# Kernel tuning notes

Hardware: AMD Instinct MI355X
Metric: run time of the kernel (lower is better)

Reference implementation:

```python
import jax, jax.numpy as jnp
import numpy as np

HEADS = 8
DIM_HEAD = 64
NB_FEATURES = 266
EPS = 1e-4


def softmax_kernel(data, projection, is_query):
    # data: (b, h, n, d); projection: (m, d)
    dn = data.shape[-1] ** -0.25                       # data normalizer d^{-1/4}
    ratio = projection.shape[0] ** -0.5                # m^{-1/2}
    dd = jnp.einsum('bhnd,md->bhnm', dn * data, projection)
    diag = (jnp.sum(data * data, axis=-1, keepdims=True) * 0.5) * (dn * dn)
    stab = jnp.max(dd, axis=-1, keepdims=True) if is_query else jnp.max(dd)
    return ratio * (jnp.exp(dd - diag - stab) + EPS)


def linear_attention(q, k, v):
    # q,k: (b,h,n,m) kernel features; v: (b,h,n,d)
    k_sum = k.sum(axis=-2)                                   # (b,h,m)
    D_inv = 1.0 / jnp.einsum('bhnm,bhm->bhn', q, k_sum)      # (b,h,n)
    context = jnp.einsum('bhnm,bhnd->bhmd', k, v)            # (b,h,m,d)
    return jnp.einsum('bhmd,bhnm,bhn->bhnd', context, q, D_inv)


def reference(x, W_qkv, W_out, projection, f):
    B, N, dim = x.shape
    h, dh = HEADS, DIM_HEAD
    qkv = x @ W_qkv                                          # (B,N,3*h*dh)
    q, k, v = jnp.split(qkv, 3, axis=-1)
    to_bh = lambda t: t.reshape(B, N, h, dh).transpose(0, 2, 1, 3).reshape(B * h, N, dh)
    q, k, v = to_bh(q), to_bh(k), to_bh(v)
    q = q * (dh ** -0.5)
    cls_q, q_ = q[:, :1], q[:, 1:]
    cls_k, k_ = k[:, :1], k[:, 1:]
    cls_v, v_ = v[:, :1], v[:, 1:]
    # cls token attends to ALL tokens with exact softmax attention
    sim = jnp.einsum('bid,bjd->bij', cls_q, k)
    cls_out = jnp.einsum('bij,bjd->bid', jax.nn.softmax(sim, axis=-1), v)
    # space attention regroup: 'b (f n) d -> (b f) n d'
    n_sp = (N - 1) // f
    grp = lambda t: t.reshape(B * h * f, n_sp, dh)
    q_, k_, v_ = grp(q_), grp(k_), grp(v_)
    # broadcast cls k/v to each group: 'b () d -> (b r) () d', r = f
    k_ = jnp.concatenate([jnp.repeat(cls_k, f, axis=0), k_], axis=1)  # (B*h*f, n_sp+1, dh)
    v_ = jnp.concatenate([jnp.repeat(cls_v, f, axis=0), v_], axis=1)
    # '(b h) f d -> b h f d'
    sh = lambda t: t.reshape(-1, h, t.shape[1], dh)
    qp = softmax_kernel(sh(q_), projection, True)
    kp = softmax_kernel(sh(k_), projection, False)
    out = linear_attention(qp, kp, sh(v_))                   # (-1, h, n_sp, dh)
    out = out.reshape(B * h, f * n_sp, dh)                   # '(b f) n d -> b (f n) d'
    out = jnp.concatenate([cls_out, out], axis=1)            # (B*h, N, dh)
    out = out.reshape(B, h, N, dh).transpose(0, 2, 1, 3).reshape(B, N, h * dh)
    return out @ W_out


def setup_inputs():
    key = jax.random.key(0)
    ks = jax.random.split(key, 3)
    B, F, S, dim = 8, 16, 196, 512
    N = 1 + F * S
    dh, m = DIM_HEAD, NB_FEATURES
    x = jax.random.normal(ks[0], (B, N, dim), dtype=jnp.float32)
    W_qkv = jax.random.normal(ks[1], (dim, 3 * dim), dtype=jnp.float32) * (dim ** -0.5)
    W_out = jax.random.normal(ks[2], (dim, dim), dtype=jnp.float32) * (dim ** -0.5)
    # gaussian orthogonal random matrix (scaling=0): QR blocks, chi-norm row scales
    rng = np.random.default_rng(0)
    blocks = []
    for _ in range(m // dh):
        qm, _ = np.linalg.qr(rng.standard_normal((dh, dh)))
        blocks.append(qm.T)
    rem = m - (m // dh) * dh
    if rem > 0:
        qm, _ = np.linalg.qr(rng.standard_normal((dh, dh)))
        blocks.append(qm.T[:rem])
    proj = np.concatenate(blocks, axis=0)
    multiplier = np.linalg.norm(rng.standard_normal((m, dh)), axis=1)
    projection = jnp.asarray(multiplier[:, None] * proj, dtype=jnp.float32)
    return {"x": x, "W_qkv": W_qkv, "W_out": W_out, "projection": projection, "f": F}
```

## Files before the change

### kernel.cpp

```cpp
#include <hip/hip_runtime.h>
#include <hip/hip_bf16.h>

namespace {

typedef __bf16 bf16x8 __attribute__((ext_vector_type(8)));
typedef float  f32x4  __attribute__((ext_vector_type(4)));
typedef unsigned short ushort8 __attribute__((ext_vector_type(8)));
typedef unsigned int u32;

constexpr int NTOK  = 3137;
constexpr int NH    = 8;
constexpr int DH    = 64;
constexpr int BH    = 64;
constexpr int MROWS = 8 * NTOK;
constexpr int NROWS = BH * NTOK;
constexpr int MF    = 266;
constexpr int MPK   = 320;
constexpr int MC    = 288;
constexpr int MS    = 320;
constexpr int NMAXB = (NROWS + 255) / 256;
constexpr int NCH   = 13;
constexpr int NBQKV = 197 * 12;
constexpr int NBOUT = 197 * 4;

constexpr float DN     = 0.35355339059327379f;
constexpr float HDN2   = 0.0625f;
constexpr float RATIO  = 0.0613139368f;
constexpr float EPSV   = 1.0e-4f;
constexpr float QSCALE = 0.125f;

__device__ __forceinline__ int swz64(int r, int c)  { return (r << 6) + (c ^ ((r & 7) << 3)); }
__device__ __forceinline__ int swz320(int r, int c) { return r * 320 + (c ^ ((r & 7) << 3)); }

__device__ __forceinline__ int xcdchunk(int bid, int nb) {
  const int q = nb >> 3, r = nb & 7;
  const int xcd = bid & 7, slot = bid >> 3;
  return (xcd < r ? xcd * (q + 1) : r * (q + 1) + (xcd - r) * q) + slot;
}

__device__ __forceinline__ float b2f(unsigned short u) {
  union { unsigned int i; float f; } cv;
  cv.i = ((unsigned int)u) << 16;
  return cv.f;
}
__device__ __forceinline__ unsigned short f2b(float f) {
  __hip_bfloat16 h = __float2bfloat16(f);
  union { __hip_bfloat16 h; unsigned short u; } cv;
  cv.h = h;
  return cv.u;
}
__device__ __forceinline__ unsigned int pk2(float a, float b) {
  return (unsigned int)f2b(a) | ((unsigned int)f2b(b) << 16);
}
__device__ __forceinline__ u32 fenc(float f) {
  u32 u = __float_as_uint(f);
  return (u & 0x80000000u) ? ~u : (u | 0x80000000u);
}
__device__ __forceinline__ float fdec(u32 u) {
  return __uint_as_float((u & 0x80000000u) ? (u ^ 0x80000000u) : ~u);
}
__device__ __forceinline__ void gload16(const void* g, void* l) {
  __builtin_amdgcn_global_load_lds(
      (const __attribute__((address_space(1))) u32*)g,
      (__attribute__((address_space(3))) u32*)l, 16, 0, 0);
}

__global__ __launch_bounds__(256) void k_projb(
    const float* __restrict__ proj, unsigned short* __restrict__ projb,
    u32* __restrict__ gmaxu)
{
  const int idx = (blockIdx.x * 256 + threadIdx.x) * 8;
  if (idx < MPK * 64) {
    const int m = idx >> 6, c0 = idx & 63;
    uint4 u;
    if (m < MF) {
      const float* src = proj + (size_t)m * 64 + c0;
      const float4 f0 = *(const float4*)src;
      const float4 f1 = *(const float4*)(src + 4);
      u.x = pk2(f0.x, f0.y); u.y = pk2(f0.z, f0.w);
      u.z = pk2(f1.x, f1.y); u.w = pk2(f1.z, f1.w);
    } else {
      u = uint4{0, 0, 0, 0};
    }
    *(uint4*)&projb[swz64(m, c0)] = u;
  }
  if (blockIdx.x == 0 && threadIdx.x == 0) *gmaxu = 0u;
}

__global__ __launch_bounds__(256) void k_cvt(
    const float* __restrict__ src, unsigned short* __restrict__ dst, int n8)
{
  const int i = blockIdx.x * 256 + threadIdx.x;
  if (i < n8) {
    const float4 f0 = *(const float4*)(src + (size_t)i * 8);
    const float4 f1 = *(const float4*)(src + (size_t)i * 8 + 4);
    uint4 u;
    u.x = pk2(f0.x, f0.y); u.y = pk2(f0.z, f0.w);
    u.z = pk2(f1.x, f1.y); u.w = pk2(f1.z, f1.w);
    *(uint4*)(dst + (size_t)i * 8) = u;
  }
}

__global__ __launch_bounds__(256) void k_tconv(
    const float* __restrict__ src, unsigned short* __restrict__ dst,
    int R, int C)
{
  __shared__ float tile[64][65];
  const int cb = blockIdx.x * 64, rb = blockIdx.y * 64;
  const int tid = threadIdx.x;
  const int tr = tid >> 4, tc4 = (tid & 15) * 4;
  #pragma unroll
  for (int i = 0; i < 4; ++i) {
    const int r = tr + i * 16;
    const float4 f = *(const float4*)(src + (size_t)(rb + r) * C + cb + tc4);
    tile[r][tc4 + 0] = f.x; tile[r][tc4 + 1] = f.y;
    tile[r][tc4 + 2] = f.z; tile[r][tc4 + 3] = f.w;
  }
  __syncthreads();
  #pragma unroll
  for (int i = 0; i < 4; ++i) {
    const int wrow = tr + i * 16;
    uint2 u;
    u.x = pk2(tile[tc4 + 0][wrow], tile[tc4 + 1][wrow]);
    u.y = pk2(tile[tc4 + 2][wrow], tile[tc4 + 3][wrow]);
    *(uint2*)&dst[(size_t)(cb + wrow) * R + rb + tc4] = u;
  }
}

__global__ __launch_bounds__(256) void k_qkv(
    const unsigned short* __restrict__ xb,
    const unsigned short* __restrict__ wT,
    unsigned short* __restrict__ qb, unsigned short* __restrict__ kb,
    unsigned short* __restrict__ vb)
{
  __shared__ alignas(16) unsigned short As[128 * 64];
  __shared__ alignas(16) unsigned short Bs[128 * 64];
  const int lid = xcdchunk(blockIdx.x, NBQKV);
  const int bm = lid / 12, bn = lid % 12;
  const int tid = threadIdx.x;
  const int lane = tid & 63, wid = tid >> 6;
  const int wr = wid >> 1, wc = wid & 1;
  const int row0 = bm * 128, col0 = bn * 128;
  const int l15 = lane & 15, l4 = lane >> 4;
  const int lr = lane >> 3;
  const int srcChunk = (lane & 7) ^ lr;

  const unsigned short* aRow[4];
  const unsigned short* bRow[4];
  #pragma unroll
  for (int j = 0; j < 4; ++j) {
    int gr = row0 + wid * 32 + j * 8 + lr;
    if (gr >= MROWS) gr = MROWS - 1;
    aRow[j] = xb + (size_t)gr * 512 + srcChunk * 8;
    bRow[j] = wT + (size_t)(col0 + wid * 32 + j * 8 + lr) * 512 + srcChunk * 8;
  }

  f32x4 acc[4][4];
  #pragma unroll
  for (int i = 0; i < 4; ++i)
    #pragma unroll
    for (int j = 0; j < 4; ++j) acc[i][j] = f32x4{0.f, 0.f, 0.f, 0.f};

  for (int kt = 0; kt < 512; kt += 64) {
    #pragma unroll
    for (int j = 0; j < 4; ++j) {
      gload16(aRow[j] + kt, &As[(wid * 32 + j * 8) * 64]);
      gload16(bRow[j] + kt, &Bs[(wid * 32 + j * 8) * 64]);
    }
    __syncthreads();
    #pragma unroll
    for (int ks = 0; ks < 2; ++ks) {
      bf16x8 af[4], bfr[4];
      #pragma unroll
      for (int i = 0; i < 4; ++i)
        af[i] = *(const bf16x8*)&As[swz64(wr * 64 + i * 16 + l15, ks * 32 + l4 * 8)];
      #pragma unroll
      for (int i = 0; i < 4; ++i)
        bfr[i] = *(const bf16x8*)&Bs[swz64(wc * 64 + i * 16 + l15, ks * 32 + l4 * 8)];
      #pragma unroll
      for (int mi = 0; mi < 4; ++mi)
        #pragma unroll
        for (int ni = 0; ni < 4; ++ni)
          acc[mi][ni] = __builtin_amdgcn_mfma_f32_16x16x32_bf16(
              af[mi], bfr[ni], acc[mi][ni], 0, 0, 0);
    }
    __syncthreads();
  }
  #pragma unroll
  for (int mi = 0; mi < 4; ++mi) {
    #pragma unroll
    for (int r = 0; r < 4; ++r) {
      const int grow = row0 + wr * 64 + mi * 16 + l4 * 4 + r;
      if (grow < MROWS) {
        const int bb = grow / NTOK, n = grow - bb * NTOK;
        #pragma unroll
        for (int ni = 0; ni < 4; ++ni) {
          const int gc = col0 + wc * 64 + ni * 16 + l15;
          const int which = gc >> 9;
          const int col = gc & 511;
          const int hh = col >> 6, d = col & 63;
          const size_t off = (size_t)((bb * NH + hh) * NTOK + n) * DH + d;
          const float vv = acc[mi][ni][r];
          if (which == 0)      qb[off] = f2b(vv * QSCALE);
          else if (which == 1) kb[off] = f2b(vv);
          else                 vb[off] = f2b(vv);
        }
      }
    }
  }
}

__global__ __launch_bounds__(256) void k_out(
    const unsigned short* __restrict__ a,
    const unsigned short* __restrict__ wT,
    float* __restrict__ out)
{
  __shared__ alignas(16) unsigned short As[128 * 64];
  __shared__ alignas(16) unsigned short Bs[128 * 64];
  const int lid = xcdchunk(blockIdx.x, NBOUT);
  const int bm = lid / 4, bn = lid % 4;
  const int tid = threadIdx.x;
  const int lane = tid & 63, wid = tid >> 6;
  const int wr = wid >> 1, wc = wid & 1;
  const int row0 = bm * 128, col0 = bn * 128;
  const int l15 = lane & 15, l4 = lane >> 4;
  const int lr = lane >> 3;
  const int srcChunk = (lane & 7) ^ lr;

  const unsigned short* aRow[4];
  const unsigned short* bRow[4];
  #pragma unroll
  for (int j = 0; j < 4; ++j) {
    int gr = row0 + wid * 32 + j * 8 + lr;
    if (gr >= MROWS) gr = MROWS - 1;
    aRow[j] = a + (size_t)gr * 512 + srcChunk * 8;
    bRow[j] = wT + (size_t)(col0 + wid * 32 + j * 8 + lr) * 512 + srcChunk * 8;
  }

  f32x4 acc[4][4];
  #pragma unroll
  for (int i = 0; i < 4; ++i)
    #pragma unroll
    for (int j = 0; j < 4; ++j) acc[i][j] = f32x4{0.f, 0.f, 0.f, 0.f};

  for (int kt = 0; kt < 512; kt += 64) {
    #pragma unroll
    for (int j = 0; j < 4; ++j) {
      gload16(aRow[j] + kt, &As[(wid * 32 + j * 8) * 64]);
      gload16(bRow[j] + kt, &Bs[(wid * 32 + j * 8) * 64]);
    }
    __syncthreads();
    #pragma unroll
    for (int ks = 0; ks < 2; ++ks) {
      bf16x8 af[4], bfr[4];
      #pragma unroll
      for (int i = 0; i < 4; ++i)
        af[i] = *(const bf16x8*)&As[swz64(wr * 64 + i * 16 + l15, ks * 32 + l4 * 8)];
      #pragma unroll
      for (int i = 0; i < 4; ++i)
        bfr[i] = *(const bf16x8*)&Bs[swz64(wc * 64 + i * 16 + l15, ks * 32 + l4 * 8)];
      #pragma unroll
      for (int mi = 0; mi < 4; ++mi)
        #pragma unroll
        for (int ni = 0; ni < 4; ++ni)
          acc[mi][ni] = __builtin_amdgcn_mfma_f32_16x16x32_bf16(
              af[mi], bfr[ni], acc[mi][ni], 0, 0, 0);
    }
    __syncthreads();
  }
  #pragma unroll
  for (int mi = 0; mi < 4; ++mi) {
    #pragma unroll
    for (int r = 0; r < 4; ++r) {
      const int grow = row0 + wr * 64 + mi * 16 + l4 * 4 + r;
      if (grow < MROWS) {
        #pragma unroll
        for (int ni = 0; ni < 4; ++ni) {
          const int gc = col0 + wc * 64 + ni * 16 + l15;
          out[(size_t)grow * 512 + gc] = acc[mi][ni][r];
        }
      }
    }
  }
}

__global__ __launch_bounds__(256) void k_cls1(
    const unsigned short* __restrict__ qb, const unsigned short* __restrict__ kb,
    float* __restrict__ simb, float* __restrict__ cmax)
{
  __shared__ float qv[64];
  __shared__ float sred[4];
  const int bh = blockIdx.x, ch = blockIdx.y, tid = threadIdx.x;
  if (tid < 64) qv[tid] = b2f(qb[(size_t)bh * NTOK * 64 + tid]);
  __syncthreads();
  const int j = ch * 256 + tid;
  float dot = -3e38f;
  if (j < NTOK) {
    const unsigned short* kr = kb + (size_t)bh * NTOK * 64 + (size_t)j * 64;
    dot = 0.f;
    #pragma unroll
    for (int d0 = 0; d0 < 64; d0 += 8) {
      const bf16x8 kv = *(const bf16x8*)(kr + d0);
      #pragma unroll
      for (int j2 = 0; j2 < 8; ++j2) dot += qv[d0 + j2] * (float)kv[j2];
    }
    simb[bh * 3200 + j] = dot;
  }
  float lm = dot;
  #pragma unroll
  for (int off = 32; off; off >>= 1) lm = fmaxf(lm, __shfl_xor(lm, off));
  if ((tid & 63) == 0) sred[tid >> 6] = lm;
  __syncthreads();
  if (tid == 0)
    cmax[bh * NCH + ch] = fmaxf(fmaxf(sred[0], sred[1]), fmaxf(sred[2], sred[3]));
}

__global__ __launch_bounds__(256) void k_cls2(
    const unsigned short* __restrict__ vb, const float* __restrict__ simb,
    const float* __restrict__ cmax, float* __restrict__ pacc,
    float* __restrict__ psum)
{
  __shared__ float pa[4][64];
  __shared__ float pw[4];
  const int bh = blockIdx.x, ch = blockIdx.y, tid = threadIdx.x;
  const int wave = tid >> 6, d = tid & 63;
  float mx = -3e38f;
  #pragma unroll
  for (int i = 0; i < NCH; ++i) mx = fmaxf(mx, cmax[bh * NCH + i]);
  float acc = 0.f, ps = 0.f;
  const int j0 = ch * 256 + wave * 64;
  for (int i = 0; i < 64; ++i) {
    const int j = j0 + i;
    if (j < NTOK) {
      const float p = __expf(simb[bh * 3200 + j] - mx);
      acc += p * b2f(vb[(size_t)bh * NTOK * 64 + (size_t)j * 64 + d]);
      ps += p;
    }
  }
  pa[wave][d] = acc;
  if (d == 0) pw[wave] = ps;
  __syncthreads();
  if (tid < 64)
    pacc[((size_t)bh * NCH + ch) * 64 + tid] = pa[0][tid] + pa[1][tid] + pa[2][tid] + pa[3][tid];
  if (tid == 0)
    psum[bh * NCH + ch] = pw[0] + pw[1] + pw[2] + pw[3];
}

__global__ __launch_bounds__(64) void k_cls3(
    const float* __restrict__ pacc, const float* __restrict__ psum,
    unsigned short* __restrict__ attnb)
{
  const int bh = blockIdx.x, d = threadIdx.x;
  float a = 0.f, s = 0.f;
  #pragma unroll
  for (int ch = 0; ch < NCH; ++ch) {
    a += pacc[((size_t)bh * NCH + ch) * 64 + d];
    s += psum[bh * NCH + ch];
  }
  const int bb = bh >> 3, hh = bh & 7;
  attnb[((size_t)bb * NTOK + 0) * 512 + hh * 64 + d] = f2b(a / s);
}

__global__ __launch_bounds__(256) void k_keymax(
    const unsigned short* __restrict__ kb, const unsigned short* __restrict__ projb,
    u32* __restrict__ gmaxu)
{
  __shared__ alignas(16) unsigned short projL[MPK * 64];
  __shared__ float red[4];
  const int blk = blockIdx.x, tid = threadIdx.x;
  const int lane = tid & 63, wave = tid >> 6;
  const int l15 = lane & 15, l4 = lane >> 4;
  const int mw0 = wave * 80;
  {
    const char* srcb = (const char*)projb;
    char* dstb = (char*)projL;
    #pragma unroll
    for (int j = 0; j < 10; ++j) {
      const int off = (j * 4 + wave) * 1024;
      gload16(srcb + off + lane * 16, dstb + off);
    }
  }
  __syncthreads();
  float lm = -3e38f;
  for (int rg = 0; rg < 4; ++rg) {
    const int row0 = (blk * 4 + rg) * 64;
    if (row0 >= NROWS) break;
    bf16x8 bfrag[4][2];
    #pragma unroll
    for (int tf = 0; tf < 4; ++tf) {
      int gr = row0 + tf * 16 + l15;
      if (gr >= NROWS) gr = NROWS - 1;
      #pragma unroll
      for (int ks = 0; ks < 2; ++ks)
        bfrag[tf][ks] = *(const bf16x8*)(kb + (size_t)gr * 64 + ks * 32 + l4 * 8);
    }
    f32x4 acc[5][4];
    #pragma unroll
    for (int i = 0; i < 5; ++i)
      #pragma unroll
      for (int j = 0; j < 4; ++j) acc[i][j] = f32x4{0.f, 0.f, 0.f, 0.f};
    #pragma unroll
    for (int mf = 0; mf < 5; ++mf) {
      const bf16x8 a0 = *(const bf16x8*)&projL[swz64(mw0 + mf * 16 + l15, l4 * 8)];
      const bf16x8 a1 = *(const bf16x8*)&projL[swz64(mw0 + mf * 16 + l15, 32 + l4 * 8)];
      #pragma unroll
      for (int tf = 0; tf < 4; ++tf) {
        acc[mf][tf] = __builtin_amdgcn_mfma_f32_16x16x32_bf16(a0, bfrag[tf][0], acc[mf][tf], 0, 0, 0);
        acc[mf][tf] = __builtin_amdgcn_mfma_f32_16x16x32_bf16(a1, bfrag[tf][1], acc[mf][tf], 0, 0, 0);
      }
    }
    #pragma unroll
    for (int tf = 0; tf < 4; ++tf) {
      const bool colok = (row0 + tf * 16 + l15) < NROWS;
      #pragma unroll
      for (int mf = 0; mf < 5; ++mf)
        #pragma unroll
        for (int r = 0; r < 4; ++r) {
          const int m = mw0 + mf * 16 + l4 * 4 + r;
          if (colok && m < MF) lm = fmaxf(lm, DN * acc[mf][tf][r]);
        }
    }
  }
  #pragma unroll
  for (int off = 32; off; off >>= 1) lm = fmaxf(lm, __shfl_xor(lm, off));
  if (lane == 0) red[wave] = lm;
  __syncthreads();
  if (tid == 0) {
    const float bm = fmaxf(fmaxf(red[0], red[1]), fmaxf(red[2], red[3]));
    atomicMax(gmaxu, fenc(bm));
  }
}

__global__ __launch_bounds__(512) void k_ctx(
    const unsigned short* __restrict__ kb, const unsigned short* __restrict__ vb,
    const unsigned short* __restrict__ projb, const u32* __restrict__ gmaxu,
    unsigned short* __restrict__ ctxg, float* __restrict__ ksumg)
{
  __shared__ alignas(16) unsigned short kpT[MC * 64];
  __shared__ alignas(16) unsigned short vT[2][64 * 64];
  __shared__ float diag_l[2][64];

  const int g = blockIdx.x, bh = g >> 4, c = g & 15;
  const int tid = threadIdx.x;
  const int lane = tid & 63, wave = tid >> 6;
  const int l15 = lane & 15, l4 = lane >> 4;
  const int nf = (wave < 2) ? 3 : 2;
  const int M0 = (wave < 2) ? wave * 48 : 96 + (wave - 2) * 32;
  const float gm = fdec(*gmaxu);

  bf16x8 pfr[3][2];
  #pragma unroll
  for (int mf = 0; mf < 3; ++mf)
    #pragma unroll
    for (int ks = 0; ks < 2; ++ks)
      pfr[mf][ks] = (mf < nf)
          ? *(const bf16x8*)&projb[swz64(M0 + mf * 16 + l15, ks * 32 + l4 * 8)]
          : bf16x8{0, 0, 0, 0, 0, 0, 0, 0};

  const unsigned short* ksrc = kb + (size_t)bh * NTOK * 64;
  const unsigned short* vsrc = vb + (size_t)bh * NTOK * 64;

  f32x4 ctxacc[3][4];
  #pragma unroll
  for (int i = 0; i < 3; ++i)
    #pragma unroll
    for (int j = 0; j < 4; ++j) ctxacc[i][j] = f32x4{0.f, 0.f, 0.f, 0.f};
  float ksump[3][4];
  #pragma unroll
  for (int i = 0; i < 3; ++i)
    #pragma unroll
    for (int j = 0; j < 4; ++j) ksump[i][j] = 0.f;

  auto stagevd = [&](int kt, int buf) {
    {
      const int t = tid & 63, dblk = (tid >> 6) & 7;
      const int n = kt * 64 + t;
      if (n < 197) {
        const int node = (n == 0) ? 0 : 1 + c * 196 + (n - 1);
        const ushort8 v = *(const ushort8*)(vsrc + (size_t)node * 64 + dblk * 8);
        #pragma unroll
        for (int j = 0; j < 8; ++j) vT[buf][swz64(dblk * 8 + j, t)] = v[j];
      } else {
        #pragma unroll
        for (int j = 0; j < 8; ++j) vT[buf][swz64(dblk * 8 + j, t)] = 0;
      }
    }
    if (tid < 64) {
      const int n = kt * 64 + tid;
      const int nn = (n < 197) ? n : 0;
      const int node = (nn == 0) ? 0 : 1 + c * 196 + (nn - 1);
      const unsigned short* kr = ksrc + (size_t)node * 64;
      float s = 0.f;
      #pragma unroll
      for (int d0 = 0; d0 < 64; d0 += 8) {
        const bf16x8 v = *(const bf16x8*)(kr + d0);
        #pragma unroll
        for (int j = 0; j < 8; ++j) { const float f = (float)v[j]; s += f * f; }
      }
      diag_l[buf][tid] = HDN2 * s;
    }
  };
  auto computef = [&](int kt, int buf) {
    #pragma unroll
    for (int tf = 0; tf < 4; ++tf) {
      const int n = kt * 64 + tf * 16 + l15;
      const int nn = (n < 197) ? n : 0;
      const int node = (nn == 0) ? 0 : 1 + c * 196 + (nn - 1);
      bf16x8 b0 = *(const bf16x8*)(ksrc + (size_t)node * 64 + l4 * 8);
      bf16x8 b1 = *(const bf16x8*)(ksrc + (size_t)node * 64 + 32 + l4 * 8);
      f32x4 a1[3];
      #pragma unroll
      for (int mf = 0; mf < 3; ++mf) {
        a1[mf] = f32x4{0.f, 0.f, 0.f, 0.f};
        if (mf < nf) {
          a1[mf] = __builtin_amdgcn_mfma_f32_16x16x32_bf16(pfr[mf][0], b0, a1[mf], 0, 0, 0);
          a1[mf] = __builtin_amdgcn_mfma_f32_16x16x32_bf16(pfr[mf][1], b1, a1[mf], 0, 0, 0);
        }
      }
      const int t = tf * 16 + l15;
      const int nv = kt * 64 + t;
      const float dg = diag_l[buf][t];
      #pragma unroll
      for (int mf = 0; mf < 3; ++mf) {
        if (mf < nf) {
          #pragma unroll
          for (int r = 0; r < 4; ++r) {
            const int m = M0 + mf * 16 + l4 * 4 + r;
            float kp = 0.f;
            if (m < MF && nv < 197)
              kp = RATIO * (__expf(DN * a1[mf][r] - dg - gm) + EPSV);
            ksump[mf][r] += kp;
            kpT[swz64(m, t)] = f2b(kp);
          }
        }
      }
    }
    #pragma unroll
    for (int ks = 0; ks < 2; ++ks) {
      bf16x8 a2[3];
      #pragma unroll
      for (int mf = 0; mf < 3; ++mf)
        if (mf < nf)
          a2[mf] = *(const bf16x8*)&kpT[swz64(M0 + mf * 16 + l15, ks * 32 + l4 * 8)];
      #pragma unroll
      for (int df = 0; df < 4; ++df) {
        const bf16x8 b2 = *(const bf16x8*)&vT[buf][swz64(df * 16 + l15, ks * 32 + l4 * 8)];
        #pragma unroll
        for (int mf = 0; mf < 3; ++mf)
          if (mf < nf)
            ctxacc[mf][df] = __builtin_amdgcn_mfma_f32_16x16x32_bf16(a2[mf], b2, ctxacc[mf][df], 0, 0, 0);
      }
    }
  };

  stagevd(0, 0);
  __syncthreads();
  for (int kt = 0; kt < 4; ++kt) {
    const int b = kt & 1;
    if (kt < 3) stagevd(kt + 1, b ^ 1);
    computef(kt, b);
    __syncthreads();
  }

  #pragma unroll
  for (int mf = 0; mf < 3; ++mf) {
    if (mf < nf) {
      #pragma unroll
      for (int r = 0; r < 4; ++r) {
        float v = ksump[mf][r];
        v += __shfl_xor(v, 1); v += __shfl_xor(v, 2);
        v += __shfl_xor(v, 4); v += __shfl_xor(v, 8);
        if (l15 == 0) ksumg[(size_t)g * MC + M0 + mf * 16 + l4 * 4 + r] = v;
      }
    }
  }
  #pragma unroll
  for (int mf = 0; mf < 3; ++mf) {
    if (mf < nf) {
      #pragma unroll
      for (int df = 0; df < 4; ++df) {
        const int d = df * 16 + l15;
        const int m = M0 + mf * 16 + l4 * 4;
        uint2 u;
        u.x = pk2(ctxacc[mf][df][0], ctxacc[mf][df][1]);
        u.y = pk2(ctxacc[mf][df][2], ctxacc[mf][df][3]);
        *(uint2*)&ctxg[(size_t)g * 64 * MS + swz320(d, m)] = u;
      }
    }
  }
}

__global__ __launch_bounds__(512) void k_qry(
    const unsigned short* __restrict__ qb, const unsigned short* __restrict__ projb,
    const unsigned short* __restrict__ ctxg, const float* __restrict__ ksumg,
    unsigned short* __restrict__ attnb)
{
  __shared__ alignas(16) unsigned short qp[2][64 * 320];
  __shared__ alignas(16) unsigned short ctxL[64 * 320];
  __shared__ float diag_l[2][64];
  __shared__ float rmax_l[2][8][64];
  __shared__ float dnm_l[2][8][64];

  const int g = blockIdx.x, bh = g >> 4, c = g & 15;
  const int bb = bh >> 3, hh = bh & 7;
  const int tid = threadIdx.x;
  const int lane = tid & 63, wave = tid >> 6;
  const int l15 = lane & 15, l4 = lane >> 4;
  const int nf = (wave < 2) ? 3 : 2;
  const int M0 = (wave < 2) ? wave * 48 : 96 + (wave - 2) * 32;

  {
    const char* srcb = (const char*)(ctxg + (size_t)g * 64 * MS);
    char* dstb = (char*)ctxL;
    #pragma unroll
    for (int j = 0; j < 5; ++j) {
      const int off = (j * 8 + wave) * 1024;
      gload16(srcb + off + lane * 16, dstb + off);
    }
  }

  bf16x8 pfr[3][2];
  #pragma unroll
  for (int mf = 0; mf < 3; ++mf)
    #pragma unroll
    for (int ks = 0; ks < 2; ++ks)
      pfr[mf][ks] = (mf < nf)
          ? *(const bf16x8*)&projb[swz64(M0 + mf * 16 + l15, ks * 32 + l4 * 8)]
          : bf16x8{0, 0, 0, 0, 0, 0, 0, 0};

  float ksr[3][4];
  #pragma unroll
  for (int mf = 0; mf < 3; ++mf) {
    if (mf < nf) {
      const float4 kv = *(const float4*)(ksumg + (size_t)g * MC + M0 + mf * 16 + l4 * 4);
      ksr[mf][0] = kv.x; ksr[mf][1] = kv.y; ksr[mf][2] = kv.z; ksr[mf][3] = kv.w;
    } else {
      ksr[mf][0] = ksr[mf][1] = ksr[mf][2] = ksr[mf][3] = 0.f;
    }
  }

  const unsigned short* qsrc = qb + (size_t)bh * NTOK * 64;
  const int tf4 = wave & 3, dfh = wave >> 2;

  auto diagf = [&](int qt, int buf) {
    if (tid < 64) {
      const int n = qt * 64 + tid;
      const int nn = (n < 196) ? n : 0;
      const int node = 1 + c * 196 + nn;
      const unsigned short* qr = qsrc + (size_t)node * 64;
      float s = 0.f;
      #pragma unroll
      for (int d0 = 0; d0 < 64; d0 += 8) {
        const bf16x8 v = *(const bf16x8*)(qr + d0);
        #pragma unroll
        for (int j = 0; j < 8; ++j) { const float f = (float)v[j]; s += f * f; }
      }
      diag_l[buf][tid] = HDN2 * s;
    }
  };
  auto stage3f = [&](int qt, int buf, f32x4 (&acc3)[3][4]) {
    #pragma unroll
    for (int i = 0; i < 3; ++i)
      #pragma unroll
      for (int j = 0; j < 4; ++j) acc3[i][j] = f32x4{0.f, 0.f, 0.f, 0.f};
    #pragma unroll
    for (int tf = 0; tf < 4; ++tf) {
      const int n = qt * 64 + tf * 16 + l15;
      const int nn = (n < 196) ? n : 0;
      const int node = 1 + c * 196 + nn;
      bf16x8 b0 = *(const bf16x8*)(qsrc + (size_t)node * 64 + l4 * 8);
      bf16x8 b1 = *(const bf16x8*)(qsrc + (size_t)node * 64 + 32 + l4 * 8);
      #pragma unroll
      for (int mf = 0; mf < 3; ++mf) {
        if (mf < nf) {
          acc3[mf][tf] = __builtin_amdgcn_mfma_f32_16x16x32_bf16(pfr[mf][0], b0, acc3[mf][tf], 0, 0, 0);
          acc3[mf][tf] = __builtin_amdgcn_mfma_f32_16x16x32_bf16(pfr[mf][1], b1, acc3[mf][tf], 0, 0, 0);
        }
      }
    }
    #pragma unroll
    for (int tf = 0; tf < 4; ++tf) {
      float v = -3e38f;
      #pragma unroll
      for (int mf = 0; mf < 3; ++mf)
        if (mf < nf)
          #pragma unroll
          for (int r = 0; r < 4; ++r) {
            const int m = M0 + mf * 16 + l4 * 4 + r;
            if (m < MF) v = fmaxf(v, DN * acc3[mf][tf][r]);
          }
      v = fmaxf(v, __shfl_xor(v, 16));
      v = fmaxf(v, __shfl_xor(v, 32));
      if (l4 == 0) rmax_l[buf][wave][tf * 16 + l15] = v;
    }
  };
  auto qpwritef = [&](int qt, int buf, const f32x4 (&acc3)[3][4]) {
    #pragma unroll
    for (int tf = 0; tf < 4; ++tf) {
      const int t = tf * 16 + l15;
      const int tq = qt * 64 + t;
      float rm = fmaxf(fmaxf(rmax_l[buf][0][t], rmax_l[buf][1][t]),
                       fmaxf(rmax_l[buf][2][t], rmax_l[buf][3][t]));
      rm = fmaxf(rm, fmaxf(fmaxf(rmax_l[buf][4][t], rmax_l[buf][5][t]),
                           fmaxf(rmax_l[buf][6][t], rmax_l[buf][7][t])));
      const float dg = diag_l[buf][t];
      float dpart = 0.f;
      #pragma unroll
      for (int mf = 0; mf < 3; ++mf) {
        if (mf < nf) {
          float e[4];
          #pragma unroll
          for (int r = 0; r < 4; ++r) {
            const int m = M0 + mf * 16 + l4 * 4 + r;
            e[r] = (m < MF && tq < 196)
                 ? RATIO * (__expf(DN * acc3[mf][tf][r] - dg - rm) + EPSV) : 0.f;
            dpart += e[r] * ksr[mf][r];
          }
          uint2 u; u.x = pk2(e[0], e[1]); u.y = pk2(e[2], e[3]);
          *(uint2*)&qp[buf][swz320(t, M0 + mf * 16 + l4 * 4)] = u;
        }
      }
      dpart += __shfl_xor(dpart, 16);
      dpart += __shfl_xor(dpart, 32);
      if (l4 == 0) dnm_l[buf][wave][t] = dpart;
    }
  };
  auto stage4f = [&](int qt, int buf) {
    f32x4 oacc[2];
    oacc[0] = f32x4{0.f, 0.f, 0.f, 0.f};
    oacc[1] = f32x4{0.f, 0.f, 0.f, 0.f};
    #pragma unroll
    for (int ks = 0; ks < 9; ++ks) {
      const bf16x8 a4 = *(const bf16x8*)&qp[buf][swz320(tf4 * 16 + l15, ks * 32 + l4 * 8)];
      #pragma unroll
      for (int di = 0; di < 2; ++di) {
        const int d = dfh * 32 + di * 16 + l15;
        const bf16x8 b4 = *(const bf16x8*)&ctxL[swz320(d, ks * 32 + l4 * 8)];
        oacc[di] = __builtin_amdgcn_mfma_f32_16x16x32_bf16(a4, b4, oacc[di], 0, 0, 0);
      }
    }
    #pragma unroll
    for (int r = 0; r < 4; ++r) {
      const int tl = tf4 * 16 + l4 * 4 + r;
      const int tq = qt * 64 + tl;
      if (tq < 196) {
        float denom = 0.f;
        #pragma unroll
        for (int w8 = 0; w8 < 8; ++w8) denom += dnm_l[buf][w8][tl];
        const float dinv = 1.0f / denom;
        const int node = 1 + c * 196 + tq;
        unsigned short* orow = attnb + ((size_t)bb * NTOK + node) * 512 + hh * 64 + dfh * 32;
        #pragma unroll
        for (int di = 0; di < 2; ++di)
          orow[di * 16 + l15] = f2b(oacc[di][r] * dinv);
      }
    }
  };

  f32x4 acc3[3][4];
  diagf(0, 0);
  stage3f(0, 0, acc3);
  __syncthreads();
  qpwritef(0, 0, acc3);
  for (int qt = 1; qt < 4; ++qt) {
    const int b = qt & 1, pb = b ^ 1;
    __syncthreads();
    diagf(qt, b);
    stage3f(qt, b, acc3);
    __syncthreads();
    stage4f(qt - 1, pb);
    qpwritef(qt, b, acc3);
  }
  __syncthreads();
  stage4f(3, 1);
}

}

extern "C" void kernel_launch(void* const* d_in, const int* in_sizes, int n_in,
                              void* d_out, int out_size, void* d_ws, size_t ws_size,
                              hipStream_t stream) {
  (void)in_sizes; (void)n_in; (void)out_size; (void)ws_size;
  const float* x    = (const float*)d_in[0];
  const float* wqkv = (const float*)d_in[1];
  const float* wout = (const float*)d_in[2];
  const float* proj = (const float*)d_in[3];
  float* out = (float*)d_out;

  const size_t QKV = (size_t)BH * NTOK * DH;
  unsigned short* qb    = (unsigned short*)d_ws;
  unsigned short* kb    = qb + QKV;
  unsigned short* vb    = kb + QKV;
  unsigned short* attnb = vb + QKV;
  float* fbase = (float*)(attnb + QKV);
  u32*   gmaxu = (u32*)(fbase + 4096);
  float* simb = fbase + 8192;
  float* cmax = simb + 64 * 3200;
  float* pacc = cmax + 1024;
  float* psum = pacc + 64 * NCH * 64;
  unsigned short* wqkvT = (unsigned short*)(psum + 1024);
  unsigned short* woutT = wqkvT + 1536 * 512;
  unsigned short* ctxg  = woutT + 512 * 512;
  float* ksumg = (float*)(ctxg + (size_t)1024 * 64 * MS);
  unsigned short* projb = (unsigned short*)(ksumg + 1024 * MC);
  unsigned short* xb = attnb;

  const dim3 blk(256);
  k_projb  <<<dim3(10),       blk, 0, stream>>>(proj, projb, gmaxu);
  k_tconv  <<<dim3(24, 8),    blk, 0, stream>>>(wqkv, wqkvT, 512, 1536);
  k_tconv  <<<dim3(8, 8),     blk, 0, stream>>>(wout, woutT, 512, 512);
  k_cvt    <<<dim3((int)(QKV / 8 + 255) / 256), blk, 0, stream>>>(x, xb, (int)(QKV / 8));
  k_qkv    <<<dim3(NBQKV),    blk, 0, stream>>>(xb, wqkvT, qb, kb, vb);
  k_cls1   <<<dim3(BH, NCH),  blk, 0, stream>>>(qb, kb, simb, cmax);
  k_cls2   <<<dim3(BH, NCH),  blk, 0, stream>>>(vb, simb, cmax, pacc, psum);
  k_cls3   <<<dim3(BH), dim3(64), 0, stream>>>(pacc, psum, attnb);
  k_keymax <<<dim3(NMAXB),    blk, 0, stream>>>(kb, projb, gmaxu);
  k_ctx    <<<dim3(1024), dim3(512), 0, stream>>>(kb, vb, projb, gmaxu, ctxg, ksumg);
  k_qry    <<<dim3(1024), dim3(512), 0, stream>>>(qb, projb, ctxg, ksumg, attnb);
  k_out    <<<dim3(NBOUT),    blk, 0, stream>>>(attnb, woutT, out);
}
```

Measured before the change: 341.4 us.

## Fuse key-context and query kernels into one linear-attention kernel

Merges k_ctx and k_qry into a single k_lin kernel, so each block keeps its context matrix and key sums in shared memory instead of writing them to global memory and reading them back. Shared memory is reused between the key-feature/V buffers and the query-feature double buffer, which raises LDS use per block and may lower occupancy. The query loop is also reordered so stage4f of the previous tile runs before stage3f of the current one.

After: 323.4 us. 1.06x faster.

```diff
diff --git a/kernel.cpp b/kernel.cpp
--- a/kernel.cpp
+++ b/kernel.cpp
@@ -17,7 +17,6 @@
 constexpr int MF    = 266;
 constexpr int MPK   = 320;
 constexpr int MC    = 288;
-constexpr int MS    = 320;
 constexpr int NMAXB = (NROWS + 255) / 256;
 constexpr int NCH   = 13;
 constexpr int NBQKV = 197 * 12;
@@ -431,16 +430,23 @@
   }
 }
 
-__global__ __launch_bounds__(512) void k_ctx(
+__global__ __launch_bounds__(512) void k_lin(
     const unsigned short* __restrict__ kb, const unsigned short* __restrict__ vb,
-    const unsigned short* __restrict__ projb, const u32* __restrict__ gmaxu,
-    unsigned short* __restrict__ ctxg, float* __restrict__ ksumg)
-{
-  __shared__ alignas(16) unsigned short kpT[MC * 64];
-  __shared__ alignas(16) unsigned short vT[2][64 * 64];
-  __shared__ float diag_l[2][64];
+    const unsigned short* __restrict__ qb, const unsigned short* __restrict__ projb,
+    const u32* __restrict__ gmaxu, unsigned short* __restrict__ attnb)
+{
+  __shared__ alignas(16) unsigned short smAB[2 * 64 * 320];
+  __shared__ alignas(16) unsigned short ctxL[64 * 320];
+  __shared__ float diagA[2][64];
+  __shared__ float diagB[2][64];
+  __shared__ float rmax_l[2][8][64];
+  __shared__ float dnm_l[2][8][64];
+
+  unsigned short* const kpT = smAB;
+  unsigned short* const vTb = smAB + MC * 64;
 
   const int g = blockIdx.x, bh = g >> 4, c = g & 15;
+  const int bb = bh >> 3, hh = bh & 7;
   const int tid = threadIdx.x;
   const int lane = tid & 63, wave = tid >> 6;
   const int l15 = lane & 15, l4 = lane >> 4;
@@ -459,6 +465,7 @@
 
   const unsigned short* ksrc = kb + (size_t)bh * NTOK * 64;
   const unsigned short* vsrc = vb + (size_t)bh * NTOK * 64;
+  const unsigned short* qsrc = qb + (size_t)bh * NTOK * 64;
 
   f32x4 ctxacc[3][4];
   #pragma unroll
@@ -475,14 +482,15 @@
     {
       const int t = tid & 63, dblk = (tid >> 6) & 7;
       const int n = kt * 64 + t;
+      unsigned short* vT = vTb + buf * 4096;
       if (n < 197) {
         const int node = (n == 0) ? 0 : 1 + c * 196 + (n - 1);
         const ushort8 v = *(const ushort8*)(vsrc + (size_t)node * 64 + dblk * 8);
         #pragma unroll
-        for (int j = 0; j < 8; ++j) vT[buf][swz64(dblk * 8 + j, t)] = v[j];
+        for (int j = 0; j < 8; ++j) vT[swz64(dblk * 8 + j, t)] = v[j];
       } else {
         #pragma unroll
-        for (int j = 0; j < 8; ++j) vT[buf][swz64(dblk * 8 + j, t)] = 0;
+        for (int j = 0; j < 8; ++j) vT[swz64(dblk * 8 + j, t)] = 0;
       }
     }
     if (tid < 64) {
@@ -497,7 +505,7 @@
         #pragma unroll
         for (int j = 0; j < 8; ++j) { const float f = (float)v[j]; s += f * f; }
       }
-      diag_l[buf][tid] = HDN2 * s;
+      diagA[buf][tid] = HDN2 * s;
     }
   };
   auto computef = [&](int kt, int buf) {
@@ -519,7 +527,7 @@
       }
       const int t = tf * 16 + l15;
       const int nv = kt * 64 + t;
-      const float dg = diag_l[buf][t];
+      const float dg = diagA[buf][t];
       #pragma unroll
       for (int mf = 0; mf < 3; ++mf) {
         if (mf < nf) {
@@ -542,9 +550,10 @@
       for (int mf = 0; mf < 3; ++mf)
         if (mf < nf)
           a2[mf] = *(const bf16x8*)&kpT[swz64(M0 + mf * 16 + l15, ks * 32 + l4 * 8)];
+      const unsigned short* vT = vTb + buf * 4096;
       #pragma unroll
       for (int df = 0; df < 4; ++df) {
-        const bf16x8 b2 = *(const bf16x8*)&vT[buf][swz64(df * 16 + l15, ks * 32 + l4 * 8)];
+        const bf16x8 b2 = *(const bf16x8*)&vT[swz64(df * 16 + l15, ks * 32 + l4 * 8)];
         #pragma unroll
         for (int mf = 0; mf < 3; ++mf)
           if (mf < nf)
@@ -562,16 +571,15 @@
     __syncthreads();
   }
 
+  float ksr[3][4];
   #pragma unroll
   for (int mf = 0; mf < 3; ++mf) {
-    if (mf < nf) {
-      #pragma unroll
-      for (int r = 0; r < 4; ++r) {
-        float v = ksump[mf][r];
-        v += __shfl_xor(v, 1); v += __shfl_xor(v, 2);
-        v += __shfl_xor(v, 4); v += __shfl_xor(v, 8);
-        if (l15 == 0) ksumg[(size_t)g * MC + M0 + mf * 16 + l4 * 4 + r] = v;
-      }
+    #pragma unroll
+    for (int r = 0; r < 4; ++r) {
+      float v = ksump[mf][r];
+      v += __shfl_xor(v, 1); v += __shfl_xor(v, 2);
+      v += __shfl_xor(v, 4); v += __shfl_xor(v, 8);
+      ksr[mf][r] = v;
     }
   }
   #pragma unroll
@@ -584,62 +592,12 @@
         uint2 u;
         u.x = pk2(ctxacc[mf][df][0], ctxacc[mf][df][1]);
         u.y = pk2(ctxacc[mf][df][2], ctxacc[mf][df][3]);
-        *(uint2*)&ctxg[(size_t)g * 64 * MS + swz320(d, m)] = u;
-      }
-    }
-  }
-}
-
-__global__ __launch_bounds__(512) void k_qry(
-    const unsigned short* __restrict__ qb, const unsigned short* __restrict__ projb,
-    const unsigned short* __restrict__ ctxg, const float* __restrict__ ksumg,
-    unsigned short* __restrict__ attnb)
-{
-  __shared__ alignas(16) unsigned short qp[2][64 * 320];
-  __shared__ alignas(16) unsigned short ctxL[64 * 320];
-  __shared__ float diag_l[2][64];
-  __shared__ float rmax_l[2][8][64];
-  __shared__ float dnm_l[2][8][64];
-
-  const int g = blockIdx.x, bh = g >> 4, c = g & 15;
-  const int bb = bh >> 3, hh = bh & 7;
-  const int tid = threadIdx.x;
-  const int lane = tid & 63, wave = tid >> 6;
-  const int l15 = lane & 15, l4 = lane >> 4;
-  const int nf = (wave < 2) ? 3 : 2;
-  const int M0 = (wave < 2) ? wave * 48 : 96 + (wave - 2) * 32;
-
-  {
-    const char* srcb = (const char*)(ctxg + (size_t)g * 64 * MS);
-    char* dstb = (char*)ctxL;
-    #pragma unroll
-    for (int j = 0; j < 5; ++j) {
-      const int off = (j * 8 + wave) * 1024;
-      gload16(srcb + off + lane * 16, dstb + off);
-    }
-  }
-
-  bf16x8 pfr[3][2];
-  #pragma unroll
-  for (int mf = 0; mf < 3; ++mf)
-    #pragma unroll
-    for (int ks = 0; ks < 2; ++ks)
-      pfr[mf][ks] = (mf < nf)
-          ? *(const bf16x8*)&projb[swz64(M0 + mf * 16 + l15, ks * 32 + l4 * 8)]
-          : bf16x8{0, 0, 0, 0, 0, 0, 0, 0};
-
-  float ksr[3][4];
-  #pragma unroll
-  for (int mf = 0; mf < 3; ++mf) {
-    if (mf < nf) {
-      const float4 kv = *(const float4*)(ksumg + (size_t)g * MC + M0 + mf * 16 + l4 * 4);
-      ksr[mf][0] = kv.x; ksr[mf][1] = kv.y; ksr[mf][2] = kv.z; ksr[mf][3] = kv.w;
-    } else {
-      ksr[mf][0] = ksr[mf][1] = ksr[mf][2] = ksr[mf][3] = 0.f;
-    }
-  }
-
-  const unsigned short* qsrc = qb + (size_t)bh * NTOK * 64;
+        *(uint2*)&ctxL[swz320(d, m)] = u;
+      }
+    }
+  }
+  __syncthreads();
+
   const int tf4 = wave & 3, dfh = wave >> 2;
 
   auto diagf = [&](int qt, int buf) {
@@ -655,7 +613,7 @@
         #pragma unroll
         for (int j = 0; j < 8; ++j) { const float f = (float)v[j]; s += f * f; }
       }
-      diag_l[buf][tid] = HDN2 * s;
+      diagB[buf][tid] = HDN2 * s;
     }
   };
   auto stage3f = [&](int qt, int buf, f32x4 (&acc3)[3][4]) {
@@ -695,6 +653,7 @@
     }
   };
   auto qpwritef = [&](int qt, int buf, const f32x4 (&acc3)[3][4]) {
+    unsigned short* qp = smAB + buf * (64 * 320);
     #pragma unroll
     for (int tf = 0; tf < 4; ++tf) {
       const int t = tf * 16 + l15;
@@ -703,7 +662,7 @@
                        fmaxf(rmax_l[buf][2][t], rmax_l[buf][3][t]));
       rm = fmaxf(rm, fmaxf(fmaxf(rmax_l[buf][4][t], rmax_l[buf][5][t]),
                            fmaxf(rmax_l[buf][6][t], rmax_l[buf][7][t])));
-      const float dg = diag_l[buf][t];
+      const float dg = diagB[buf][t];
       float dpart = 0.f;
       #pragma unroll
       for (int mf = 0; mf < 3; ++mf) {
@@ -717,7 +676,7 @@
             dpart += e[r] * ksr[mf][r];
           }
           uint2 u; u.x = pk2(e[0], e[1]); u.y = pk2(e[2], e[3]);
-          *(uint2*)&qp[buf][swz320(t, M0 + mf * 16 + l4 * 4)] = u;
+          *(uint2*)&qp[swz320(t, M0 + mf * 16 + l4 * 4)] = u;
         }
       }
       dpart += __shfl_xor(dpart, 16);
@@ -726,12 +685,13 @@
     }
   };
   auto stage4f = [&](int qt, int buf) {
+    const unsigned short* qp = smAB + buf * (64 * 320);
     f32x4 oacc[2];
     oacc[0] = f32x4{0.f, 0.f, 0.f, 0.f};
     oacc[1] = f32x4{0.f, 0.f, 0.f, 0.f};
     #pragma unroll
     for (int ks = 0; ks < 9; ++ks) {
-      const bf16x8 a4 = *(const bf16x8*)&qp[buf][swz320(tf4 * 16 + l15, ks * 32 + l4 * 8)];
+      const bf16x8 a4 = *(const bf16x8*)&qp[swz320(tf4 * 16 + l15, ks * 32 + l4 * 8)];
       #pragma unroll
       for (int di = 0; di < 2; ++di) {
         const int d = dfh * 32 + di * 16 + l15;
@@ -766,9 +726,9 @@
     const int b = qt & 1, pb = b ^ 1;
     __syncthreads();
     diagf(qt, b);
+    stage4f(qt - 1, pb);
     stage3f(qt, b, acc3);
     __syncthreads();
-    stage4f(qt - 1, pb);
     qpwritef(qt, b, acc3);
   }
   __syncthreads();
@@ -800,9 +760,7 @@
   float* psum = pacc + 64 * NCH * 64;
   unsigned short* wqkvT = (unsigned short*)(psum + 1024);
   unsigned short* woutT = wqkvT + 1536 * 512;
-  unsigned short* ctxg  = woutT + 512 * 512;
-  float* ksumg = (float*)(ctxg + (size_t)1024 * 64 * MS);
-  unsigned short* projb = (unsigned short*)(ksumg + 1024 * MC);
+  unsigned short* projb = woutT + 512 * 512;
   unsigned short* xb = attnb;
 
   const dim3 blk(256);
@@ -815,7 +773,6 @@
   k_cls2   <<<dim3(BH, NCH),  blk, 0, stream>>>(vb, simb, cmax, pacc, psum);
   k_cls3   <<<dim3(BH), dim3(64), 0, stream>>>(pacc, psum, attnb);
   k_keymax <<<dim3(NMAXB),    blk, 0, stream>>>(kb, projb, gmaxu);
-  k_ctx    <<<dim3(1024), dim3(512), 0, stream>>>(kb, vb, projb, gmaxu, ctxg, ksumg);
-  k_qry    <<<dim3(1024), dim3(512), 0, stream>>>(qb, projb, ctxg, ksumg, attnb);
+  k_lin    <<<dim3(1024), dim3(512), 0, stream>>>(kb, vb, qb, projb, gmaxu, attnb);
   k_out    <<<dim3(NBOUT),    blk, 0, stream>>>(attnb, woutT, out);
 }
```
